# Optimization experiments

Measured on AMD Instinct MI355X. Metric: run time of the kernel, lower is better.

The kernel has to match this reference:

```python
import jax, jax.numpy as jnp
import numpy as np

H = 16          # bit depth; n = 2**H
K = 4           # f*H // division_fact = 2*16//8
TP = 8          # number of coordinate copies
N = 1 << H
T1 = 128        # query block
T2 = 512        # key block
D = 256         # euclidean embedding dim
C = 2 * K * H + 1  # connection candidates = 129


def _distance(c1, c2, norm):
    # sign/exponent 'critical graph' distance:
    # sg = sign(c1)*sign(c2); s = frexp_exponent(|c1|^|c2| + 1)/H
    sg = ((2 * (c1 >= 0).astype(jnp.int32) - 1) *
          (2 * (c2 >= 0).astype(jnp.int32) - 1)).astype(jnp.float32)
    xr = jnp.abs(c1) ^ jnp.abs(c2)
    _, e = jnp.frexp((xr + 1).astype(jnp.float32))
    return sg * (1.0 - e.astype(jnp.float32) / H) * norm


def setup_inputs() -> dict:
    key = jax.random.key(0)
    k1, k2, k3, k4, k5, k6 = jax.random.split(key, 6)
    emb_T1 = jax.random.normal(k1, (T1, D), jnp.float32)
    emb_T2 = jax.random.normal(k2, (T2, D), jnp.float32)
    # locations are signed integers in [1-n, n) as in __init__
    sta_loc = jax.random.randint(k3, (T1, TP), 1 - N, N, jnp.int32)
    pos_loc = jax.random.randint(k4, (T2, TP), 1 - N, N, jnp.int32)
    # neighbor valid_mask: choosing_mask = rand > 0.2
    mask = jax.random.bernoulli(k5, 0.8, (T1, T2))
    # raw random numbers for generate_random_masks (low-bit masks applied inside reference)
    random_masks = jax.random.randint(k6, (T1, H, K, TP), 0, N, jnp.int32)
    return {"emb_T1": emb_T1, "emb_T2": emb_T2, "sta_loc": sta_loc,
            "pos_loc": pos_loc, "mask": mask, "random_masks": random_masks}


def reference(emb_T1, emb_T2, sta_loc, pos_loc, mask, random_masks):
    # ---- connection(): bit-flip XOR candidate generation ----
    flip = (jnp.int32(1) << jnp.arange(H, dtype=jnp.int32))          # (H,)
    flipped = sta_loc[:, None, :] ^ flip[None, :, None]              # (T1, H, TP)
    low = random_masks & (flip - 1)[None, :, None, None]             # keep low i bits
    res = (flipped[:, :, None, :] ^ low).reshape(T1, H * K, TP)      # (T1, H*K, TP)
    cnc_loc = jnp.concatenate([res, sta_loc[:, None, :], -res], axis=1)  # (T1, C, TP)

    # ---- normalized_matmul -> target similarity val_v; val_n = ones ----
    e1 = emb_T1 / jnp.linalg.norm(emb_T1, axis=-1, keepdims=True)
    e2 = emb_T2 / jnp.linalg.norm(emb_T2, axis=-1, keepdims=True)
    val_v = e1 @ e2.T                                                # (T1, T2)

    # ---- distances (val_n == 1) ----
    dis_sta = _distance(sta_loc[:, None, :], pos_loc[None, :, :], 1.0)       # (T1,T2,TP)
    dsum = dis_sta.sum(-1)                                                   # (T1,T2)
    dis_cnc = _distance(cnc_loc[:, None, :, :], pos_loc[None, :, None, :], 1.0)  # (T1,T2,C,TP)
    ct_val = (dsum[:, :, None, None] - dis_sta[:, :, None, :] + dis_cnc) / TP    # (T1,T2,C,TP)

    # ---- masked MSE loss, summed over the T2 (neighbor) dim ----
    diff = ct_val - val_v[:, :, None, None]
    loss = (diff * diff * mask[:, :, None, None].astype(jnp.float32)).sum(axis=1)  # (T1,C,TP)
    return loss
```

## Files before the change

### kernel.cpp

```cpp
#include <hip/hip_runtime.h>
#include <stdint.h>

#define T1c 128
#define T2c 512
#define TPc 8
#define Cc  129
#define Dc  256
#define ST  64
#define MBS 68

__device__ __forceinline__ int pack_loc(int v) {
    int a = v < 0 ? -v : v;
    return a | (v < 0 ? (int)0x80000000 : 0);
}

__device__ __forceinline__ void dist_core(unsigned v1, unsigned v2, float& dd, float& val) {
    unsigned xv = v1 ^ v2;
    val = fmaf((float)__clz((int)((xv & 0x7FFFFFFFu) + 1u)), 0.0625f, -1.0f);
    dd  = __uint_as_float(__float_as_uint(val) ^ (xv & 0x80000000u));
}

__device__ __forceinline__ float wave_sum(float v) {
    #pragma unroll
    for (int off = 32; off; off >>= 1) v += __shfl_xor(v, off, 64);
    return v;
}

__global__ __launch_bounds__(256, 4) void k_fused(
    const float* __restrict__ e1, const float* __restrict__ e2,
    const int* __restrict__ sta, const int* __restrict__ pos,
    const void* __restrict__ mask, const int* __restrict__ rm,
    float* __restrict__ out) {
    int b  = blockIdx.x;
    int t1 = b >> 3;
    int s  = b & 7;
    int base = s * ST;
    int tid  = threadIdx.x;

    __shared__ float se1[Dc];
    __shared__ float sdot[256], sss[256];
    __shared__ float smbs[TPc][MBS];
    __shared__ int   spp[TPc][MBS];
    __shared__ float sA[TPc], sSb[TPc];
    __shared__ float sSm, sC64, sinv1;
    __shared__ int   sflag;

    if (tid == 0) sflag = 0;
    __syncthreads();
    {
        bool nz = ((const unsigned char*)mask)[1 + 4 * tid] != 0;
        if (__any(nz) && (tid & 63) == 0) sflag = 1;
    }
    if (tid < 64) {
        float4 a = ((const float4*)(e1 + (size_t)t1 * Dc))[tid];
        ((float4*)se1)[tid] = a;
        float ssum = wave_sum(a.x * a.x + a.y * a.y + a.z * a.z + a.w * a.w);
        if (tid == 0) sinv1 = rsqrtf(ssum);
    }
    __syncthreads();

    {
        int t2 = base + (tid >> 2), h = tid & 3;
        const float4* xrow = (const float4*)(e2 + (size_t)t2 * Dc) + h * 16;
        const float4* arow = (const float4*)se1 + h * 16;
        float dx = 0.f, dy = 0.f, dz = 0.f, dw = 0.f;
        float sx = 0.f, sy = 0.f, sz = 0.f, sw = 0.f;
        #pragma unroll
        for (int d = 0; d < 16; ++d) {
            float4 x = xrow[d];
            float4 a = arow[d];
            dx = fmaf(a.x, x.x, dx); dy = fmaf(a.y, x.y, dy);
            dz = fmaf(a.z, x.z, dz); dw = fmaf(a.w, x.w, dw);
            sx = fmaf(x.x, x.x, sx); sy = fmaf(x.y, x.y, sy);
            sz = fmaf(x.z, x.z, sz); sw = fmaf(x.w, x.w, sw);
        }
        sdot[tid] = (dx + dy) + (dz + dw);
        sss[tid]  = (sx + sy) + (sz + sw);
    }
    __syncthreads();

    if (tid < ST) {
        int t2 = base + tid;
        float dot = (sdot[4 * tid] + sdot[4 * tid + 1]) + (sdot[4 * tid + 2] + sdot[4 * tid + 3]);
        float ss  = (sss[4 * tid]  + sss[4 * tid + 1])  + (sss[4 * tid + 2]  + sss[4 * tid + 3]);
        float vv  = dot * sinv1 * rsqrtf(ss);
        int idx = t1 * T2c + t2;
        float m;
        if (sflag) m = (((const unsigned char*)mask)[idx] != 0) ? 1.0f : 0.0f;
        else       m = (((const int*)mask)[idx] != 0) ? 1.0f : 0.0f;

        int4 p0 = ((const int4*)(pos + (size_t)t2 * TPc))[0];
        int4 p1 = ((const int4*)(pos + (size_t)t2 * TPc))[1];
        int pk[8] = {pack_loc(p0.x), pack_loc(p0.y), pack_loc(p0.z), pack_loc(p0.w),
                     pack_loc(p1.x), pack_loc(p1.y), pack_loc(p1.z), pack_loc(p1.w)};
        int4 s0 = ((const int4*)(sta + (size_t)t1 * TPc))[0];
        int4 s1 = ((const int4*)(sta + (size_t)t1 * TPc))[1];
        int sk[8] = {pack_loc(s0.x), pack_loc(s0.y), pack_loc(s0.z), pack_loc(s0.w),
                     pack_loc(s1.x), pack_loc(s1.y), pack_loc(s1.z), pack_loc(s1.w)};
        float d[8];
        float dsum = 0.f;
        #pragma unroll
        for (int p = 0; p < 8; ++p) {
            float dd, val;
            dist_core((unsigned)sk[p], (unsigned)pk[p], dd, val);
            d[p] = dd;
            dsum += dd;
        }
        float accA[8], accSb[8];
        #pragma unroll
        for (int p = 0; p < 8; ++p) {
            float mb  = m * ((dsum - d[p]) * 0.125f - vv);
            float mbs = __uint_as_float(__float_as_uint(mb) ^ ((unsigned)pk[p] & 0x80000000u));
            smbs[p][tid] = mbs;
            spp[p][tid]  = (m != 0.0f) ? (pk[p] & 0x7FFFFFFF) : (int)0xFFFC0000;
            accA[p]  = mb * mb;
            accSb[p] = mbs;
        }
        float c6 = dsum * 0.125f - vv;
        float cA = m * c6 * c6;
        #pragma unroll
        for (int p = 0; p < 8; ++p) {
            accA[p]  = wave_sum(accA[p]);
            accSb[p] = wave_sum(accSb[p]);
        }
        float sm = wave_sum(m);
        cA = wave_sum(cA);
        if (tid == 0) {
            #pragma unroll
            for (int p = 0; p < 8; ++p) { sA[p] = accA[p]; sSb[p] = accSb[p]; }
            sSm = sm;
            sC64 = cA;
        }
    }
    __syncthreads();

    int p  = tid & 7;
    int c0 = tid >> 3;
    int stav = sta[t1 * TPc + p];
    int resv[2];
    unsigned v1m[2];
    #pragma unroll
    for (int k = 0; k < 2; ++k) {
        int c = c0 + 32 * k;
        int i = c >> 2, kk = c & 3;
        int low = rm[(((t1 * 16 + i) * 4 + kk) * TPc) + p] & ((1 << i) - 1);
        int rv  = (stav ^ (1 << i)) ^ low;
        resv[k] = rv;
        v1m[k]  = (unsigned)(rv < 0 ? -rv : rv);
    }

    const int4*   pp4 = (const int4*)&spp[p][0];
    const float4* mb4 = (const float4*)&smbs[p][0];

    float B0 = 0.f, B1 = 0.f, Qa0 = 0.f, Qa1 = 0.f, Qb0 = 0.f, Qb1 = 0.f;
    #pragma unroll 4
    for (int j = 0; j < 16; ++j) {
        int4   pv = pp4[j];
        float4 mb = mb4[j];
        #define EV(CMP) { \
            unsigned x0 = v1m[0] ^ (unsigned)pv.CMP; \
            unsigned x1 = v1m[1] ^ (unsigned)pv.CMP; \
            float f0 = (float)__clz((int)(x0 + 1u)); \
            float f1 = (float)__clz((int)(x1 + 1u)); \
            B0 = fmaf(mb.CMP, f0, B0); B1 = fmaf(mb.CMP, f1, B1); \
            Qa0 += f0; Qa1 += f1; \
            Qb0 = fmaf(f0, f0, Qb0); Qb1 = fmaf(f1, f1, Qb1); }
        EV(x) EV(y) EV(z) EV(w)
        #undef EV
    }

    float A = sA[p], Sb = sSb[p], Sm = sSm;
    float* o = out + (size_t)t1 * Cc * TPc;
    #pragma unroll
    for (int k = 0; k < 2; ++k) {
        int c = c0 + 32 * k;
        float Bk = (k == 0) ? B0 : B1;
        float Qak = (k == 0) ? Qa0 : Qa1;
        float Qbk = (k == 0) ? Qb0 : Qb1;
        float Bv = fmaf(Bk, 0.0625f, -Sb);
        float Bs = (resv[k] < 0) ? -Bv : Bv;
        float Qv = fmaf(Qbk, 1.0f / 256.0f, fmaf(Qak, -0.125f, Sm));
        float core = fmaf(Qv, 1.0f / 64.0f, A);
        float l0 = fmaf(Bs,  0.25f, core);
        float l1 = (resv[k] == 0) ? l0 : fmaf(Bs, -0.25f, core);
        atomicAdd(&o[c * TPc + p], l0);
        atomicAdd(&o[(65 + c) * TPc + p], l1);
    }
    if (tid < 8) atomicAdd(&o[64 * TPc + tid], sC64);
}

extern "C" void kernel_launch(void* const* d_in, const int* in_sizes, int n_in,
                              void* d_out, int out_size, void* d_ws, size_t ws_size,
                              hipStream_t stream) {
    const float* emb1 = (const float*)d_in[0];
    const float* emb2 = (const float*)d_in[1];
    const int*   sta  = (const int*)d_in[2];
    const int*   pos  = (const int*)d_in[3];
    const void*  mask = d_in[4];
    const int*   rm   = (const int*)d_in[5];

    hipLaunchKernelGGL(k_fused, dim3(1024), dim3(256), 0, stream,
                       emb1, emb2, sta, pos, mask, rm, (float*)d_out);
}
```

Baseline: 78.58 us.

## Spread per-key distance and reduction work across all 256 threads

```diff
diff --git a/kernel.cpp b/kernel.cpp
--- a/kernel.cpp
+++ b/kernel.cpp
@@ -38,9 +38,10 @@
     int tid  = threadIdx.x;
 
     __shared__ float se1[Dc];
-    __shared__ float sdot[256], sss[256];
     __shared__ float smbs[TPc][MBS];
     __shared__ int   spp[TPc][MBS];
+    __shared__ float sred[4][20];
+    __shared__ float sred2[4][2];
     __shared__ float sA[TPc], sSb[TPc];
     __shared__ float sSm, sC64, sinv1;
     __shared__ int   sflag;
@@ -60,7 +61,8 @@
     __syncthreads();
 
     {
-        int t2 = base + (tid >> 2), h = tid & 3;
+        int t2l = tid >> 2, h = tid & 3;
+        int t2 = base + t2l;
         const float4* xrow = (const float4*)(e2 + (size_t)t2 * Dc) + h * 16;
         const float4* arow = (const float4*)se1 + h * 16;
         float dx = 0.f, dy = 0.f, dz = 0.f, dw = 0.f;
@@ -74,63 +76,77 @@
             sx = fmaf(x.x, x.x, sx); sy = fmaf(x.y, x.y, sy);
             sz = fmaf(x.z, x.z, sz); sw = fmaf(x.w, x.w, sw);
         }
-        sdot[tid] = (dx + dy) + (dz + dw);
-        sss[tid]  = (sx + sy) + (sz + sw);
-    }
-    __syncthreads();
-
-    if (tid < ST) {
-        int t2 = base + tid;
-        float dot = (sdot[4 * tid] + sdot[4 * tid + 1]) + (sdot[4 * tid + 2] + sdot[4 * tid + 3]);
-        float ss  = (sss[4 * tid]  + sss[4 * tid + 1])  + (sss[4 * tid + 2]  + sss[4 * tid + 3]);
-        float vv  = dot * sinv1 * rsqrtf(ss);
+        float dq = (dx + dy) + (dz + dw);
+        float sq = (sx + sy) + (sz + sw);
+        dq += __shfl_xor(dq, 1, 64); dq += __shfl_xor(dq, 2, 64);
+        sq += __shfl_xor(sq, 1, 64); sq += __shfl_xor(sq, 2, 64);
+        float vv = dq * sinv1 * rsqrtf(sq);
+
         int idx = t1 * T2c + t2;
         float m;
         if (sflag) m = (((const unsigned char*)mask)[idx] != 0) ? 1.0f : 0.0f;
         else       m = (((const int*)mask)[idx] != 0) ? 1.0f : 0.0f;
 
-        int4 p0 = ((const int4*)(pos + (size_t)t2 * TPc))[0];
-        int4 p1 = ((const int4*)(pos + (size_t)t2 * TPc))[1];
-        int pk[8] = {pack_loc(p0.x), pack_loc(p0.y), pack_loc(p0.z), pack_loc(p0.w),
-                     pack_loc(p1.x), pack_loc(p1.y), pack_loc(p1.z), pack_loc(p1.w)};
-        int4 s0 = ((const int4*)(sta + (size_t)t1 * TPc))[0];
-        int4 s1 = ((const int4*)(sta + (size_t)t1 * TPc))[1];
-        int sk[8] = {pack_loc(s0.x), pack_loc(s0.y), pack_loc(s0.z), pack_loc(s0.w),
-                     pack_loc(s1.x), pack_loc(s1.y), pack_loc(s1.z), pack_loc(s1.w)};
-        float d[8];
-        float dsum = 0.f;
+        int2 pr = ((const int2*)(pos + (size_t)t2 * TPc))[h];
+        int2 sr = ((const int2*)(sta + (size_t)t1 * TPc))[h];
+        int pk0 = pack_loc(pr.x), pk1 = pack_loc(pr.y);
+        int sk0 = pack_loc(sr.x), sk1 = pack_loc(sr.y);
+        float d0, d1, vdead;
+        dist_core((unsigned)sk0, (unsigned)pk0, d0, vdead);
+        dist_core((unsigned)sk1, (unsigned)pk1, d1, vdead);
+        float ps = d0 + d1;
+        ps += __shfl_xor(ps, 1, 64); ps += __shfl_xor(ps, 2, 64);
+        float dsum = ps;
+
+        float mb0 = m * ((dsum - d0) * 0.125f - vv);
+        float mb1 = m * ((dsum - d1) * 0.125f - vv);
+        float mbs0 = __uint_as_float(__float_as_uint(mb0) ^ ((unsigned)pk0 & 0x80000000u));
+        float mbs1 = __uint_as_float(__float_as_uint(mb1) ^ ((unsigned)pk1 & 0x80000000u));
+        int p0 = 2 * h, p1 = 2 * h + 1;
+        smbs[p0][t2l] = mbs0;
+        smbs[p1][t2l] = mbs1;
+        spp[p0][t2l] = (m != 0.0f) ? (pk0 & 0x7FFFFFFF) : (int)0xFFFC0000;
+        spp[p1][t2l] = (m != 0.0f) ? (pk1 & 0x7FFFFFFF) : (int)0xFFFC0000;
+
+        float c6 = dsum * 0.125f - vv;
+        float aA0 = mb0 * mb0, aA1 = mb1 * mb1;
+        float aS0 = mbs0,      aS1 = mbs1;
+        float aM = (h == 0) ? m : 0.f;
+        float aC = (h == 0) ? m * c6 * c6 : 0.f;
         #pragma unroll
-        for (int p = 0; p < 8; ++p) {
-            float dd, val;
-            dist_core((unsigned)sk[p], (unsigned)pk[p], dd, val);
-            d[p] = dd;
-            dsum += dd;
-        }
-        float accA[8], accSb[8];
+        for (int off = 4; off < 64; off <<= 1) {
+            aA0 += __shfl_xor(aA0, off, 64);
+            aA1 += __shfl_xor(aA1, off, 64);
+            aS0 += __shfl_xor(aS0, off, 64);
+            aS1 += __shfl_xor(aS1, off, 64);
+            aM  += __shfl_xor(aM,  off, 64);
+            aC  += __shfl_xor(aC,  off, 64);
+        }
+        if ((tid & 63) < 4) {
+            int w = tid >> 6;
+            sred[w][h * 4 + 0] = aA0;
+            sred[w][h * 4 + 1] = aA1;
+            sred[w][h * 4 + 2] = aS0;
+            sred[w][h * 4 + 3] = aS1;
+            if (h == 0) { sred2[w][0] = aM; sred2[w][1] = aC; }
+        }
+    }
+    __syncthreads();
+
+    if (tid < 8) {
+        int h = tid >> 1, o = tid & 1;
+        float a = 0.f, bb = 0.f;
         #pragma unroll
-        for (int p = 0; p < 8; ++p) {
-            float mb  = m * ((dsum - d[p]) * 0.125f - vv);
-            float mbs = __uint_as_float(__float_as_uint(mb) ^ ((unsigned)pk[p] & 0x80000000u));
-            smbs[p][tid] = mbs;
-            spp[p][tid]  = (m != 0.0f) ? (pk[p] & 0x7FFFFFFF) : (int)0xFFFC0000;
-            accA[p]  = mb * mb;
-            accSb[p] = mbs;
-        }
-        float c6 = dsum * 0.125f - vv;
-        float cA = m * c6 * c6;
-        #pragma unroll
-        for (int p = 0; p < 8; ++p) {
-            accA[p]  = wave_sum(accA[p]);
-            accSb[p] = wave_sum(accSb[p]);
-        }
-        float sm = wave_sum(m);
-        cA = wave_sum(cA);
-        if (tid == 0) {
-            #pragma unroll
-            for (int p = 0; p < 8; ++p) { sA[p] = accA[p]; sSb[p] = accSb[p]; }
-            sSm = sm;
-            sC64 = cA;
-        }
+        for (int w = 0; w < 4; ++w) {
+            a  += sred[w][h * 4 + o];
+            bb += sred[w][h * 4 + 2 + o];
+        }
+        sA[tid]  = a;
+        sSb[tid] = bb;
+    } else if (tid == 8) {
+        sSm = sred2[0][0] + sred2[1][0] + sred2[2][0] + sred2[3][0];
+    } else if (tid == 9) {
+        sC64 = sred2[0][1] + sred2[1][1] + sred2[2][1] + sred2[3][1];
     }
     __syncthreads();
 
```

Result: no change. 79.42 us (+1.1%).
